# Performance work log

Hardware: AMD Instinct MI355X
Metric: run time of the kernel (lower is better)

The kernel has to match this reference:

```python
import jax, jax.numpy as jnp
import numpy as np

N_NODES = 100000
N_EDGES = 1600000
D_IN = 64
D_H = 64


def setup_inputs() -> dict:
    key = jax.random.key(0)
    ks = jax.random.split(key, 8)
    inp = {
        "in_feat": jax.random.normal(ks[0], (N_NODES, D_IN), dtype=jnp.float32),
        "src": jax.random.randint(ks[1], (N_EDGES,), 0, N_NODES, dtype=jnp.int64)
        if jax.config.jax_enable_x64
        else jax.random.randint(ks[1], (N_EDGES,), 0, N_NODES).astype(jnp.int32),
        "dst": jax.random.randint(ks[2], (N_EDGES,), 0, N_NODES).astype(jnp.int32),
        "W_self1": jax.random.normal(ks[3], (D_H, D_IN), dtype=jnp.float32) * 0.1,
        "W_neigh1": jax.random.normal(ks[4], (D_H, D_IN), dtype=jnp.float32) * 0.1,
        "b1": jnp.zeros((D_H,), dtype=jnp.float32),
        "W_self2": jax.random.normal(ks[5], (D_H, D_H), dtype=jnp.float32) * 0.1,
        "W_neigh2": jax.random.normal(ks[6], (D_H, D_H), dtype=jnp.float32) * 0.1,
        "b2": jnp.zeros((D_H,), dtype=jnp.float32),
    }
    inp["src"] = inp["src"].astype(jnp.int32)
    return inp


def _sage_mean(x, src, dst, W_self, W_neigh, b, n_nodes):
    # mean aggregation over incoming edges: gather src feats, segment-sum at dst
    msg_sum = jax.ops.segment_sum(x[src], dst, num_segments=n_nodes)  # [N, D]
    deg = jax.ops.segment_sum(jnp.ones_like(dst, dtype=x.dtype), dst, num_segments=n_nodes)
    h_neigh = msg_sum / jnp.maximum(deg, 1.0)[:, None]
    # DGL SAGEConv: fc_self(h) + fc_neigh(h_neigh) + bias
    return x @ W_self.T + h_neigh @ W_neigh.T + b


def reference(in_feat, src, dst, W_self1, W_neigh1, b1, W_self2, W_neigh2, b2):
    n = in_feat.shape[0]
    h = _sage_mean(in_feat, src, dst, W_self1, W_neigh1, b1, n)
    # dropout in eval mode is identity; then relu
    h = jax.nn.relu(h)
    h = _sage_mean(h, src, dst, W_self2, W_neigh2, b2, n)
    return h
```

## Files before the change

### kernel.cpp

```cpp
#include <hip/hip_runtime.h>

#define NN 100000
#define NE 1600000
#define NPAD 100352
#define NROWS 100096
#define NBKT 391
#define SENT NBKT
#define EPB 4096
#define NSB 391
#define CAST_BLKS 6250
#define WCAT_BLKS 64
#define MAXB 6144

typedef __attribute__((ext_vector_type(8))) short short8;
typedef __attribute__((ext_vector_type(4))) float float4v;

__device__ inline unsigned short f2bf(float f)
{
    union { float f; unsigned u; } v; v.f = f;
    unsigned r = v.u + 0x7FFF + ((v.u >> 16) & 1);
    return (unsigned short)(r >> 16);
}
__device__ inline float bf2f(unsigned short h)
{
    union { unsigned u; float f; } v; v.u = ((unsigned)h) << 16; return v.f;
}

__global__ __launch_bounds__(256) void prep_kernel(
    const float* __restrict__ x,
    const float* __restrict__ Ws1, const float* __restrict__ Wn1,
    const float* __restrict__ Ws2, const float* __restrict__ Wn2,
    const int* __restrict__ dst,
    unsigned short* __restrict__ XF,
    unsigned short* __restrict__ W1, unsigned short* __restrict__ W2,
    int* __restrict__ bdeg)
{
    __shared__ int lh[NBKT];
    const int b = blockIdx.x;
    if (b < CAST_BLKS) {
        int t = b * 256 + threadIdx.x;
        int n = t >> 4;
        int k4 = (t & 15) * 4;
        float4 v = *(const float4*)(x + (size_t)n * 64 + k4);
        ushort4 o;
        o.x = f2bf(v.x); o.y = f2bf(v.y); o.z = f2bf(v.z); o.w = f2bf(v.w);
        *(ushort4*)(XF + (size_t)n * 64 + k4) = o;
    } else if (b < CAST_BLKS + NSB) {
        int sb = b - CAST_BLKS;
        for (int i = threadIdx.x; i < NBKT; i += 256) lh[i] = 0;
        __syncthreads();
        int base = sb * EPB;
        int end = min(base + EPB, NE);
        for (int e = base + threadIdx.x; e < end; e += 256)
            atomicAdd(&lh[dst[e] >> 8], 1);
        __syncthreads();
        for (int i = threadIdx.x; i < NBKT; i += 256) {
            int c = lh[i];
            if (c) atomicAdd(&bdeg[i], c);
        }
    } else if (b < CAST_BLKS + NSB + WCAT_BLKS) {
        int id = (b - CAST_BLKS - NSB) * 256 + threadIdx.x;
        int l = id >> 13;
        int r = id & 8191;
        int o = r >> 7, k = r & 127;
        const float* Ws = l ? Ws2 : Ws1;
        const float* Wn = l ? Wn2 : Wn1;
        float v = (k < 64) ? Ws[o * 64 + k] : Wn[o * 64 + (k - 64)];
        (l ? W2 : W1)[r] = f2bf(v);
    } else {
        if (threadIdx.x < 16) {
            ushort4 z; z.x = 0; z.y = 0; z.z = 0; z.w = 0;
            *(ushort4*)(XF + (size_t)NN * 64 + threadIdx.x * 4) = z;
        }
    }
}

__global__ __launch_bounds__(512) void scatter_kernel(
    const int* __restrict__ src, const int* __restrict__ dst,
    const int* __restrict__ bdeg, int* __restrict__ bcur,
    int* __restrict__ colb)
{
    __shared__ int lh[NBKT];
    __shared__ int sc[512];
    __shared__ int ex[512];
    const int tid = threadIdx.x;

    for (int i = tid; i < NBKT; i += 512) lh[i] = 0;
    __syncthreads();
    int base = blockIdx.x * EPB;
    int end = min(base + EPB, NE);
    for (int e = base + tid; e < end; e += 512)
        atomicAdd(&lh[dst[e] >> 8], 1);

    int initd = bdeg[SENT];
    int v = (tid < NBKT) ? (int)((unsigned)bdeg[tid] - (unsigned)initd) : 0;
    sc[tid] = v;
    __syncthreads();
    #pragma unroll
    for (int off = 1; off < 512; off <<= 1) {
        int u = (tid >= off) ? sc[tid - off] : 0;
        __syncthreads();
        sc[tid] += u;
        __syncthreads();
    }
    ex[tid] = sc[tid] - v;
    __syncthreads();

    int initc = bcur[SENT];
    for (int i = tid; i < NBKT; i += 512) {
        int c = lh[i];
        if (c) {
            int old = atomicAdd(&bcur[i], c);
            lh[i] = ex[i] + (int)((unsigned)old - (unsigned)initc);
        }
    }
    __syncthreads();
    for (int e = base + tid; e < end; e += 512) {
        int d = dst[e];
        int p = atomicAdd(&lh[d >> 8], 1);
        colb[p] = (src[e] << 8) | (d & 255);
    }
}

__global__ __launch_bounds__(512) void fill_kernel(
    const int* __restrict__ bdeg, int* __restrict__ colb,
    int* __restrict__ rowptr)
{
    __shared__ int eb[MAXB];
    __shared__ int sc[512];
    __shared__ int cnt[256];
    __shared__ int bb[2];
    const int tid = threadIdx.x;
    const int b = blockIdx.x;

    int initd = bdeg[SENT];
    int v = (tid < NBKT) ? (int)((unsigned)bdeg[tid] - (unsigned)initd) : 0;
    sc[tid] = v;
    __syncthreads();
    #pragma unroll
    for (int off = 1; off < 512; off <<= 1) {
        int u = (tid >= off) ? sc[tid - off] : 0;
        __syncthreads();
        sc[tid] += u;
        __syncthreads();
    }
    if (tid == b) { bb[0] = sc[tid] - v; bb[1] = v; }
    __syncthreads();
    const int beg = bb[0];
    const int m = min(bb[1], MAXB);

    for (int r = tid; r < m; r += 512) eb[r] = colb[beg + r];
    if (tid < 256) cnt[tid] = 0;
    __syncthreads();
    for (int r = tid; r < m; r += 512)
        atomicAdd(&cnt[eb[r] & 255], 1);
    __syncthreads();

    int v2 = (tid < 256) ? cnt[tid] : 0;
    sc[tid] = (tid < 256) ? v2 : 0;
    __syncthreads();
    #pragma unroll
    for (int off = 1; off < 256; off <<= 1) {
        int u = (tid >= off && tid < 256) ? sc[tid - off] : 0;
        __syncthreads();
        if (tid < 256) sc[tid] += u;
        __syncthreads();
    }
    if (tid < 256) {
        int nodebase = beg + sc[tid] - v2;
        rowptr[b * 256 + tid] = nodebase;
        cnt[tid] = nodebase;
    }
    __syncthreads();

    for (int r = tid; r < m; r += 512) {
        int pk = eb[r];
        int pos = atomicAdd(&cnt[pk & 255], 1);
        colb[pos] = (pk >> 8) << 6;
    }
}

template <int LAYER1>
__global__ __launch_bounds__(256) void aggdense_kernel(
    const unsigned short* __restrict__ XIN,
    const int* __restrict__ rowptr,
    const int* __restrict__ colb,
    unsigned short* __restrict__ HN,
    const unsigned short* __restrict__ Wcat,
    const float* __restrict__ bias,
    unsigned short* __restrict__ xout,
    float* __restrict__ fout)
{
    const int tid = threadIdx.x;
    const int wave = tid >> 6;
    const int lane = tid & 63;
    const int g = lane >> 4;
    const int q = lane & 15;
    const int ZOFF = NN * 64;
    const int nbase = blockIdx.x * 64 + wave * 16;

    for (int i = 0; i < 16; ++i) {
        int n = nbase + i;
        if (n < NN) {
            int beg = rowptr[n], end = rowptr[n + 1];
            float a0 = 0.f, a1 = 0.f, a2 = 0.f, a3 = 0.f;
            for (int j = beg; j < end; j += 64) {
                int cnt = min(end - j, 64);
                int ci = (lane < cnt) ? colb[j + lane] : ZOFF;
                for (int t = 0; t < cnt; t += 16) {
                    int i0 = __shfl(ci, t + g, 64);
                    int i1 = __shfl(ci, t + 4 + g, 64);
                    int i2 = __shfl(ci, t + 8 + g, 64);
                    int i3 = __shfl(ci, t + 12 + g, 64);
                    ushort4 v0 = *(const ushort4*)(XIN + i0 + q * 4);
                    ushort4 v1 = *(const ushort4*)(XIN + i1 + q * 4);
                    ushort4 v2 = *(const ushort4*)(XIN + i2 + q * 4);
                    ushort4 v3 = *(const ushort4*)(XIN + i3 + q * 4);
                    a0 += bf2f(v0.x) + bf2f(v1.x) + bf2f(v2.x) + bf2f(v3.x);
                    a1 += bf2f(v0.y) + bf2f(v1.y) + bf2f(v2.y) + bf2f(v3.y);
                    a2 += bf2f(v0.z) + bf2f(v1.z) + bf2f(v2.z) + bf2f(v3.z);
                    a3 += bf2f(v0.w) + bf2f(v1.w) + bf2f(v2.w) + bf2f(v3.w);
                }
            }
            a0 += __shfl_xor(a0, 16, 64); a0 += __shfl_xor(a0, 32, 64);
            a1 += __shfl_xor(a1, 16, 64); a1 += __shfl_xor(a1, 32, 64);
            a2 += __shfl_xor(a2, 16, 64); a2 += __shfl_xor(a2, 32, 64);
            a3 += __shfl_xor(a3, 16, 64); a3 += __shfl_xor(a3, 32, 64);
            float rdeg = 1.0f / fmaxf((float)(end - beg), 1.0f);
            if (g == 0) {
                ushort4 o;
                o.x = f2bf(a0 * rdeg); o.y = f2bf(a1 * rdeg);
                o.z = f2bf(a2 * rdeg); o.w = f2bf(a3 * rdeg);
                *(ushort4*)(HN + (size_t)n * 64 + q * 4) = o;
            }
        }
    }
    __syncthreads();

    const int mrow = lane & 15;
    const int kb = lane >> 4;
    const int row0 = nbase;

    short8 a[4];
    {
        const short* ax = (const short*)XIN + (size_t)(row0 + mrow) * 64 + kb * 8;
        const short* ah = (const short*)HN + (size_t)(row0 + mrow) * 64 + kb * 8;
        a[0] = *(const short8*)(ax);
        a[1] = *(const short8*)(ax + 32);
        a[2] = *(const short8*)(ah);
        a[3] = *(const short8*)(ah + 32);
    }

    float4v acc[4];
    #pragma unroll
    for (int c = 0; c < 4; ++c) acc[c] = (float4v){0.f, 0.f, 0.f, 0.f};

    #pragma unroll
    for (int c = 0; c < 4; ++c) {
        const short* brow = (const short*)Wcat + (c * 16 + mrow) * 128 + kb * 8;
        #pragma unroll
        for (int i = 0; i < 4; ++i) {
            short8 bfr = *(const short8*)(brow + i * 32);
            acc[c] = __builtin_amdgcn_mfma_f32_16x16x32_bf16(a[i], bfr, acc[c], 0, 0, 0);
        }
    }

    const int rbase = row0 + (lane >> 4) * 4;
    #pragma unroll
    for (int c = 0; c < 4; ++c) {
        int o = c * 16 + mrow;
        float bv = bias[o];
        #pragma unroll
        for (int r = 0; r < 4; ++r) {
            int node = rbase + r;
            float val = acc[c][r] + bv;
            if (LAYER1) {
                float h = (node < NN) ? fmaxf(val, 0.f) : 0.f;
                xout[(size_t)node * 64 + o] = f2bf(h);
            } else {
                if (node < NN) fout[(size_t)node * 64 + o] = val;
            }
        }
    }
}

extern "C" void kernel_launch(void* const* d_in, const int* in_sizes, int n_in,
                              void* d_out, int out_size, void* d_ws, size_t ws_size,
                              hipStream_t stream)
{
    const float* in_feat = (const float*)d_in[0];
    const int*   src     = (const int*)d_in[1];
    const int*   dst     = (const int*)d_in[2];
    const float* Ws1     = (const float*)d_in[3];
    const float* Wn1     = (const float*)d_in[4];
    const float* b1      = (const float*)d_in[5];
    const float* Ws2     = (const float*)d_in[6];
    const float* Wn2     = (const float*)d_in[7];
    const float* b2      = (const float*)d_in[8];
    float* out = (float*)d_out;

    int* bdeg   = (int*)d_ws;
    int* bcur   = bdeg + 512;
    int* rowptr = bcur + 512;
    int* colb   = rowptr + NPAD;
    unsigned short* XF = (unsigned short*)(colb + NE);
    unsigned short* HN = XF + (size_t)NROWS * 64;
    unsigned short* H1 = HN + (size_t)NROWS * 64;
    unsigned short* W1 = H1 + (size_t)NROWS * 64;
    unsigned short* W2 = W1 + 8192;

    prep_kernel<<<CAST_BLKS + NSB + WCAT_BLKS + 1, 256, 0, stream>>>(
        in_feat, Ws1, Wn1, Ws2, Wn2, dst, XF, W1, W2, bdeg);

    scatter_kernel<<<NSB, 512, 0, stream>>>(src, dst, bdeg, bcur, colb);

    fill_kernel<<<NBKT, 512, 0, stream>>>(bdeg, colb, rowptr);

    const int blocks = NROWS / 64;

    aggdense_kernel<1><<<blocks, 256, 0, stream>>>(
        XF, rowptr, colb, HN, W1, b1, H1, nullptr);

    aggdense_kernel<0><<<blocks, 256, 0, stream>>>(
        H1, rowptr, colb, HN, W2, b2, nullptr, out);
}
```

Before: 250.6 us.

## Merge CSR build kernels into one cooperative kernel and prefetch next row's edges

Folds the prep, scatter and fill kernels into a single cooperative kernel of 391 blocks, using grid-wide syncs in place of kernel boundaries. The bf16 cast is spread as a grid-stride loop across those blocks. The local dst histogram for each block is kept in shared memory across phases, so dst is read one time fewer. In the aggregation kernel, each wave loads its 17 rowptr entries at once and prefetches the next node's first 64 column indices while accumulating the current node. The cost is two grid syncs and fewer blocks doing the cast, which could lower bandwidth in that phase. The larger shared-memory footprint per block may also limit occupancy for the cooperative launch.

```diff
diff --git a/kernel.cpp b/kernel.cpp
--- a/kernel.cpp
+++ b/kernel.cpp
@@ -1,4 +1,7 @@
 #include <hip/hip_runtime.h>
+#include <hip/hip_cooperative_groups.h>
+
+namespace cg = cooperative_groups;
 
 #define NN 100000
 #define NE 1600000
@@ -7,9 +10,6 @@
 #define NBKT 391
 #define SENT NBKT
 #define EPB 4096
-#define NSB 391
-#define CAST_BLKS 6250
-#define WCAT_BLKS 64
 #define MAXB 6144
 
 typedef __attribute__((ext_vector_type(8))) short short8;
@@ -26,71 +26,64 @@
     union { unsigned u; float f; } v; v.u = ((unsigned)h) << 16; return v.f;
 }
 
-__global__ __launch_bounds__(256) void prep_kernel(
+__global__ __launch_bounds__(512) void coop_build_kernel(
+    const int* __restrict__ src, const int* __restrict__ dst,
     const float* __restrict__ x,
     const float* __restrict__ Ws1, const float* __restrict__ Wn1,
     const float* __restrict__ Ws2, const float* __restrict__ Wn2,
-    const int* __restrict__ dst,
     unsigned short* __restrict__ XF,
     unsigned short* __restrict__ W1, unsigned short* __restrict__ W2,
-    int* __restrict__ bdeg)
-{
+    int* __restrict__ bdeg, int* __restrict__ bcur,
+    int* __restrict__ colb, int* __restrict__ rowptr)
+{
+    cg::grid_group grid = cg::this_grid();
     __shared__ int lh[NBKT];
+    __shared__ int sc[512];
+    __shared__ int ex[512];
+    __shared__ int eb[MAXB];
+    __shared__ int cnt[256];
+    __shared__ int bb2[2];
+
+    const int tid = threadIdx.x;
     const int b = blockIdx.x;
-    if (b < CAST_BLKS) {
-        int t = b * 256 + threadIdx.x;
+    const int base = b * EPB;
+    const int bend = min(base + EPB, NE);
+
+    for (int i = tid; i < NBKT; i += 512) lh[i] = 0;
+    __syncthreads();
+    for (int e = base + tid; e < bend; e += 512)
+        atomicAdd(&lh[dst[e] >> 8], 1);
+
+    for (int t = b * 512 + tid; t < NN * 16; t += NBKT * 512) {
         int n = t >> 4;
         int k4 = (t & 15) * 4;
         float4 v = *(const float4*)(x + (size_t)n * 64 + k4);
         ushort4 o;
         o.x = f2bf(v.x); o.y = f2bf(v.y); o.z = f2bf(v.z); o.w = f2bf(v.w);
         *(ushort4*)(XF + (size_t)n * 64 + k4) = o;
-    } else if (b < CAST_BLKS + NSB) {
-        int sb = b - CAST_BLKS;
-        for (int i = threadIdx.x; i < NBKT; i += 256) lh[i] = 0;
-        __syncthreads();
-        int base = sb * EPB;
-        int end = min(base + EPB, NE);
-        for (int e = base + threadIdx.x; e < end; e += 256)
-            atomicAdd(&lh[dst[e] >> 8], 1);
-        __syncthreads();
-        for (int i = threadIdx.x; i < NBKT; i += 256) {
-            int c = lh[i];
-            if (c) atomicAdd(&bdeg[i], c);
-        }
-    } else if (b < CAST_BLKS + NSB + WCAT_BLKS) {
-        int id = (b - CAST_BLKS - NSB) * 256 + threadIdx.x;
-        int l = id >> 13;
-        int r = id & 8191;
-        int o = r >> 7, k = r & 127;
-        const float* Ws = l ? Ws2 : Ws1;
-        const float* Wn = l ? Wn2 : Wn1;
-        float v = (k < 64) ? Ws[o * 64 + k] : Wn[o * 64 + (k - 64)];
-        (l ? W2 : W1)[r] = f2bf(v);
-    } else {
-        if (threadIdx.x < 16) {
+    }
+    if (b == 0) {
+        for (int id = tid; id < 16384; id += 512) {
+            int l = id >> 13;
+            int r = id & 8191;
+            int o = r >> 7, k = r & 127;
+            const float* Ws = l ? Ws2 : Ws1;
+            const float* Wn = l ? Wn2 : Wn1;
+            float v = (k < 64) ? Ws[o * 64 + k] : Wn[o * 64 + (k - 64)];
+            (l ? W2 : W1)[r] = f2bf(v);
+        }
+        if (tid < 16) {
             ushort4 z; z.x = 0; z.y = 0; z.z = 0; z.w = 0;
-            *(ushort4*)(XF + (size_t)NN * 64 + threadIdx.x * 4) = z;
-        }
-    }
-}
-
-__global__ __launch_bounds__(512) void scatter_kernel(
-    const int* __restrict__ src, const int* __restrict__ dst,
-    const int* __restrict__ bdeg, int* __restrict__ bcur,
-    int* __restrict__ colb)
-{
-    __shared__ int lh[NBKT];
-    __shared__ int sc[512];
-    __shared__ int ex[512];
-    const int tid = threadIdx.x;
-
-    for (int i = tid; i < NBKT; i += 512) lh[i] = 0;
-    __syncthreads();
-    int base = blockIdx.x * EPB;
-    int end = min(base + EPB, NE);
-    for (int e = base + tid; e < end; e += 512)
-        atomicAdd(&lh[dst[e] >> 8], 1);
+            *(ushort4*)(XF + (size_t)NN * 64 + tid * 4) = z;
+        }
+    }
+    __syncthreads();
+    for (int i = tid; i < NBKT; i += 512) {
+        int c = lh[i];
+        if (c) atomicAdd(&bdeg[i], c);
+    }
+    __threadfence();
+    grid.sync();
 
     int initd = bdeg[SENT];
     int v = (tid < NBKT) ? (int)((unsigned)bdeg[tid] - (unsigned)initd) : 0;
@@ -115,39 +108,18 @@
         }
     }
     __syncthreads();
-    for (int e = base + tid; e < end; e += 512) {
+    for (int e = base + tid; e < bend; e += 512) {
         int d = dst[e];
         int p = atomicAdd(&lh[d >> 8], 1);
         colb[p] = (src[e] << 8) | (d & 255);
     }
-}
-
-__global__ __launch_bounds__(512) void fill_kernel(
-    const int* __restrict__ bdeg, int* __restrict__ colb,
-    int* __restrict__ rowptr)
-{
-    __shared__ int eb[MAXB];
-    __shared__ int sc[512];
-    __shared__ int cnt[256];
-    __shared__ int bb[2];
-    const int tid = threadIdx.x;
-    const int b = blockIdx.x;
-
-    int initd = bdeg[SENT];
-    int v = (tid < NBKT) ? (int)((unsigned)bdeg[tid] - (unsigned)initd) : 0;
-    sc[tid] = v;
-    __syncthreads();
-    #pragma unroll
-    for (int off = 1; off < 512; off <<= 1) {
-        int u = (tid >= off) ? sc[tid - off] : 0;
-        __syncthreads();
-        sc[tid] += u;
-        __syncthreads();
-    }
-    if (tid == b) { bb[0] = sc[tid] - v; bb[1] = v; }
-    __syncthreads();
-    const int beg = bb[0];
-    const int m = min(bb[1], MAXB);
+    __threadfence();
+    grid.sync();
+
+    if (tid == b) { bb2[0] = ex[tid]; bb2[1] = sc[tid] - ex[tid]; }
+    __syncthreads();
+    const int beg = bb2[0];
+    const int m = min(bb2[1], MAXB);
 
     for (int r = tid; r < m; r += 512) eb[r] = colb[beg + r];
     if (tid < 256) cnt[tid] = 0;
@@ -172,7 +144,6 @@
         cnt[tid] = nodebase;
     }
     __syncthreads();
-
     for (int r = tid; r < m; r += 512) {
         int pk = eb[r];
         int pos = atomicAdd(&cnt[pk & 255], 1);
@@ -199,19 +170,51 @@
     const int ZOFF = NN * 64;
     const int nbase = blockIdx.x * 64 + wave * 16;
 
+    int rp = 0;
+    if (lane < 17) rp = rowptr[nbase + lane];
+
+    int beg = __shfl(rp, 0, 64);
+    int end = __shfl(rp, 1, 64);
+    if (nbase >= NN) { beg = 0; end = 0; }
+    int cnt0 = min(end - beg, 64);
+    int ci = (lane < cnt0) ? colb[beg + lane] : ZOFF;
+
     for (int i = 0; i < 16; ++i) {
-        int n = nbase + i;
+        const int n = nbase + i;
+        const int begC = beg, endC = end, cntC = cnt0;
+        const int ciC = ci;
+        if (i < 15) {
+            int b1 = __shfl(rp, i + 1, 64);
+            int e1 = __shfl(rp, i + 2, 64);
+            if (n + 1 >= NN) { b1 = 0; e1 = 0; }
+            beg = b1; end = e1;
+            cnt0 = min(e1 - b1, 64);
+            ci = (lane < cnt0) ? colb[b1 + lane] : ZOFF;
+        }
         if (n < NN) {
-            int beg = rowptr[n], end = rowptr[n + 1];
             float a0 = 0.f, a1 = 0.f, a2 = 0.f, a3 = 0.f;
-            for (int j = beg; j < end; j += 64) {
-                int cnt = min(end - j, 64);
-                int ci = (lane < cnt) ? colb[j + lane] : ZOFF;
-                for (int t = 0; t < cnt; t += 16) {
-                    int i0 = __shfl(ci, t + g, 64);
-                    int i1 = __shfl(ci, t + 4 + g, 64);
-                    int i2 = __shfl(ci, t + 8 + g, 64);
-                    int i3 = __shfl(ci, t + 12 + g, 64);
+            for (int t = 0; t < cntC; t += 16) {
+                int i0 = __shfl(ciC, t + g, 64);
+                int i1 = __shfl(ciC, t + 4 + g, 64);
+                int i2 = __shfl(ciC, t + 8 + g, 64);
+                int i3 = __shfl(ciC, t + 12 + g, 64);
+                ushort4 v0 = *(const ushort4*)(XIN + i0 + q * 4);
+                ushort4 v1 = *(const ushort4*)(XIN + i1 + q * 4);
+                ushort4 v2 = *(const ushort4*)(XIN + i2 + q * 4);
+                ushort4 v3 = *(const ushort4*)(XIN + i3 + q * 4);
+                a0 += bf2f(v0.x) + bf2f(v1.x) + bf2f(v2.x) + bf2f(v3.x);
+                a1 += bf2f(v0.y) + bf2f(v1.y) + bf2f(v2.y) + bf2f(v3.y);
+                a2 += bf2f(v0.z) + bf2f(v1.z) + bf2f(v2.z) + bf2f(v3.z);
+                a3 += bf2f(v0.w) + bf2f(v1.w) + bf2f(v2.w) + bf2f(v3.w);
+            }
+            for (int j = begC + 64; j < endC; j += 64) {
+                int cc = min(endC - j, 64);
+                int ci2 = (lane < cc) ? colb[j + lane] : ZOFF;
+                for (int t = 0; t < cc; t += 16) {
+                    int i0 = __shfl(ci2, t + g, 64);
+                    int i1 = __shfl(ci2, t + 4 + g, 64);
+                    int i2 = __shfl(ci2, t + 8 + g, 64);
+                    int i3 = __shfl(ci2, t + 12 + g, 64);
                     ushort4 v0 = *(const ushort4*)(XIN + i0 + q * 4);
                     ushort4 v1 = *(const ushort4*)(XIN + i1 + q * 4);
                     ushort4 v2 = *(const ushort4*)(XIN + i2 + q * 4);
@@ -226,7 +229,7 @@
             a1 += __shfl_xor(a1, 16, 64); a1 += __shfl_xor(a1, 32, 64);
             a2 += __shfl_xor(a2, 16, 64); a2 += __shfl_xor(a2, 32, 64);
             a3 += __shfl_xor(a3, 16, 64); a3 += __shfl_xor(a3, 32, 64);
-            float rdeg = 1.0f / fmaxf((float)(end - beg), 1.0f);
+            float rdeg = 1.0f / fmaxf((float)(endC - begC), 1.0f);
             if (g == 0) {
                 ushort4 o;
                 o.x = f2bf(a0 * rdeg); o.y = f2bf(a1 * rdeg);
@@ -309,12 +312,14 @@
     unsigned short* W1 = H1 + (size_t)NROWS * 64;
     unsigned short* W2 = W1 + 8192;
 
-    prep_kernel<<<CAST_BLKS + NSB + WCAT_BLKS + 1, 256, 0, stream>>>(
-        in_feat, Ws1, Wn1, Ws2, Wn2, dst, XF, W1, W2, bdeg);
-
-    scatter_kernel<<<NSB, 512, 0, stream>>>(src, dst, bdeg, bcur, colb);
-
-    fill_kernel<<<NBKT, 512, 0, stream>>>(bdeg, colb, rowptr);
+    void* args[] = {
+        (void*)&src, (void*)&dst, (void*)&in_feat,
+        (void*)&Ws1, (void*)&Wn1, (void*)&Ws2, (void*)&Wn2,
+        (void*)&XF, (void*)&W1, (void*)&W2,
+        (void*)&bdeg, (void*)&bcur, (void*)&colb, (void*)&rowptr
+    };
+    hipLaunchCooperativeKernel((void*)coop_build_kernel,
+                               dim3(NBKT), dim3(512), args, 0, stream);
 
     const int blocks = NROWS / 64;
 
```

New measurement: 557.5 us. 2.22x slower.
